# Optimization experiments

Hardware: AMD Instinct MI355X
Metric: run time of the kernel (lower is better)

The kernel has to match this reference:

```python
import jax, jax.numpy as jnp
import numpy as np

N = 50000   # nodes
E = 800000  # edges
IN, H1, H2, OUT = 128, 256, 128, 1


def setup_inputs() -> dict:
    key = jax.random.key(0)
    ks = jax.random.split(key, 9)
    x = jax.random.normal(ks[0], (N, IN), dtype=jnp.float32)
    edge_index = jax.random.randint(ks[1], (2, E), 0, N, dtype=jnp.int32)
    def glorot(k, fan_in, fan_out):
        s = np.sqrt(6.0 / (fan_in + fan_out)).astype(np.float32)
        return jax.random.uniform(k, (fan_in, fan_out), jnp.float32, -s, s)
    W1 = glorot(ks[2], IN, H1)
    b1 = jnp.zeros((H1,), jnp.float32)
    W2 = glorot(ks[3], H1, H2)
    b2 = jnp.zeros((H2,), jnp.float32)
    W3 = glorot(ks[4], H2, OUT)
    b3 = jnp.zeros((OUT,), jnp.float32)
    return {"x": x, "edge_index": edge_index, "W1": W1, "b1": b1,
            "W2": W2, "b2": b2, "W3": W3, "b3": b3}


def _gcn_layer(x, W, b, src, dst, norm):
    # dense transform [N, d_in] @ [d_in, d_out]
    h = x @ W
    # degree-normalized sparse aggregation: out[dst] += norm * h[src]
    agg = jax.ops.segment_sum(h[src] * norm[:, None], dst, num_segments=N)
    return agg + b


def reference(x, edge_index, W1, b1, W2, b2, W3, b3):
    src, dst = edge_index[0], edge_index[1]
    # PyG GCNConv: add self loops, then symmetric normalization
    loop = jnp.arange(N, dtype=src.dtype)
    src = jnp.concatenate([src, loop])
    dst = jnp.concatenate([dst, loop])
    deg = jax.ops.segment_sum(jnp.ones_like(dst, jnp.float32), dst, num_segments=N)
    dis = jax.lax.rsqrt(jnp.maximum(deg, 1.0))  # deg >= 1 via self loops
    norm = dis[src] * dis[dst]  # [E+N]
    h1 = jax.nn.relu(_gcn_layer(x, W1, b1, src, dst, norm))
    h2 = jax.nn.relu(_gcn_layer(h1, W2, b2, src, dst, norm))
    y = _gcn_layer(h2, W3, b3, src, dst, norm).reshape(-1)
    return (y, h1, h2)
```

## Files before the change

### kernel.cpp

```cpp
#include <hip/hip_runtime.h>


typedef __attribute__((ext_vector_type(8))) short short8;
typedef __attribute__((ext_vector_type(4))) float f32x4;

static __device__ __forceinline__ unsigned short f2bf(float f){
  union { float f; unsigned u; } v; v.f = f;
  unsigned r = v.u + 0x7FFF + ((v.u >> 16) & 1);
  return (unsigned short)(r >> 16);
}
static __device__ __forceinline__ float2 bf2f2(unsigned u){
  union { unsigned u; float f; } a, b;
  a.u = u << 16; b.u = u & 0xffff0000u;
  return make_float2(a.f, b.f);
}

__global__ void k_prep(const float* __restrict__ W1, const float* __restrict__ W2,
                       unsigned short* __restrict__ Wf1, unsigned short* __restrict__ Wf2,
                       const float4* __restrict__ x, uint2* __restrict__ xb, int nv,
                       int* __restrict__ bcur){
  int blk = blockIdx.x;
  int tid = threadIdx.x;
  if (blk < 256){
    if (blk == 0) bcur[tid] = 0;
    int t = blk*256 + tid;
    if (t < 32768){
      int j = t & 7, lane = (t>>3) & 63, kt = (t>>9) & 3, nt = t >> 11;
      int nn = nt*16 + (lane & 15);
      int kk = kt*32 + (lane>>4)*8 + j;
      Wf1[t] = f2bf(W1[kk*256 + nn]);
    } else {
      int o = t - 32768;
      int j = o & 7, lane = (o>>3) & 63, nt = (o>>9) & 7, kt = o >> 12;
      int nn = nt*16 + (lane & 15);
      int kk = kt*32 + (lane>>4)*8 + j;
      Wf2[o] = f2bf(W2[kk*128 + nn]);
    }
  } else {
    int i = (blk - 256)*256 + tid;
    if (i < nv){
      float4 v = x[i];
      xb[i] = make_uint2((unsigned)f2bf(v.x) | ((unsigned)f2bf(v.y) << 16),
                         (unsigned)f2bf(v.z) | ((unsigned)f2bf(v.w) << 16));
    }
  }
}

__global__ __launch_bounds__(256) void k_bin(
    const int* __restrict__ src, const int* __restrict__ dst,
    int* __restrict__ bcur, unsigned* __restrict__ pairs, int E){
  __shared__ int cl[256];
  int t = threadIdx.x;
  int e0 = blockIdx.x * 4096 + t;
  cl[t] = 0; __syncthreads();
  #pragma unroll
  for (int i = 0; i < 16; i++){
    int e = e0 + i*256;
    if (e < E) atomicAdd(&cl[dst[e] >> 8], 1);
  }
  __syncthreads();
  int c = cl[t];
  int g = (c > 0) ? atomicAdd(&bcur[t], c) : 0;
  cl[t] = g;
  __syncthreads();
  #pragma unroll
  for (int i = 0; i < 16; i++){
    int e = e0 + i*256;
    if (e < E){
      int d = dst[e];
      int b = d >> 8;
      int p = atomicAdd(&cl[b], 1);
      pairs[(b << 13) + p] = (unsigned)src[e] | ((unsigned)(d & 255) << 16);
    }
  }
}

__global__ __launch_bounds__(256) void k_place(
    const int* __restrict__ bcur, const unsigned* __restrict__ pairs,
    unsigned short* __restrict__ csr_src, int* __restrict__ rowptr,
    int* __restrict__ cnt, float* __restrict__ dis, int n, int nb){
  __shared__ int sh[256];
  __shared__ int ncnt[256];
  int t = threadIdx.x;
  int b = blockIdx.x;
  int v = (t < nb) ? bcur[t] : 0;
  sh[t] = v; __syncthreads();
  for (int off = 1; off < 256; off <<= 1){
    int x = (t >= off) ? sh[t-off] : 0;
    __syncthreads(); sh[t] += x; __syncthreads();
  }
  int csr_base = (b == 0) ? 0 : sh[b-1];
  int cnt_b = bcur[b];
  ncnt[t] = 0; __syncthreads();
  const unsigned* P = pairs + ((size_t)b << 13);
  for (int i = t; i < cnt_b; i += 256) atomicAdd(&ncnt[P[i] >> 16], 1);
  __syncthreads();
  int c = ncnt[t];
  sh[t] = c; __syncthreads();
  for (int off = 1; off < 256; off <<= 1){
    int x = (t >= off) ? sh[t-off] : 0;
    __syncthreads(); sh[t] += x; __syncthreads();
  }
  int noff = sh[t] - c;
  int node = (b << 8) + t;
  if (node < n){
    rowptr[node] = csr_base + noff;
    cnt[node] = c;
    dis[node] = rsqrtf((float)(c + 1));
  }
  ncnt[t] = noff; __syncthreads();
  for (int i = t; i < cnt_b; i += 256){
    unsigned u = P[i];
    int p = atomicAdd(&ncnt[u >> 16], 1);
    csr_src[csr_base + p] = (unsigned short)(u & 0xffff);
  }
}

__global__ void k_aggL1(const unsigned* __restrict__ xb, unsigned* __restrict__ out,
                        const int* __restrict__ rowptr, const int* __restrict__ cnt,
                        const unsigned short* __restrict__ csr_src,
                        const float* __restrict__ dis, int n){
  int t = threadIdx.x;
  int lane = t & 63;
  int node = blockIdx.x*4 + (t >> 6);
  if (node >= n) return;
  float di = dis[node];
  float2 v = bf2f2(xb[(size_t)node*64 + lane]);
  float2 acc = make_float2(di*v.x, di*v.y);
  int start = rowptr[node];
  int mm = cnt[node];
  int j = 0;
  for (; j + 15 < mm; j += 16){
    int s[16]; unsigned uv[16]; float w[16];
    #pragma unroll
    for (int q = 0; q < 16; q++) s[q] = csr_src[start+j+q];
    #pragma unroll
    for (int q = 0; q < 16; q++){ w[q] = dis[s[q]]; uv[q] = xb[(size_t)s[q]*64 + lane]; }
    #pragma unroll
    for (int q = 0; q < 16; q++){
      float2 u = bf2f2(uv[q]);
      acc.x = fmaf(w[q], u.x, acc.x); acc.y = fmaf(w[q], u.y, acc.y);
    }
  }
  for (; j + 3 < mm; j += 4){
    int s[4]; unsigned uv[4]; float w[4];
    #pragma unroll
    for (int q = 0; q < 4; q++) s[q] = csr_src[start+j+q];
    #pragma unroll
    for (int q = 0; q < 4; q++){ w[q] = dis[s[q]]; uv[q] = xb[(size_t)s[q]*64 + lane]; }
    #pragma unroll
    for (int q = 0; q < 4; q++){
      float2 u = bf2f2(uv[q]);
      acc.x = fmaf(w[q], u.x, acc.x); acc.y = fmaf(w[q], u.y, acc.y);
    }
  }
  for (; j < mm; j++){
    int s = csr_src[start+j];
    float2 u = bf2f2(xb[(size_t)s*64 + lane]);
    float w = dis[s];
    acc.x = fmaf(w, u.x, acc.x); acc.y = fmaf(w, u.y, acc.y);
  }
  acc.x *= di; acc.y *= di;
  out[(size_t)node*64 + lane] =
      (unsigned)f2bf(acc.x) | ((unsigned)f2bf(acc.y) << 16);
}

__global__ void k_aggL2(const unsigned* __restrict__ t2b, float* __restrict__ h2,
                        const int* __restrict__ rowptr, const int* __restrict__ cnt,
                        const unsigned short* __restrict__ csr_src,
                        const float* __restrict__ dis,
                        const float* __restrict__ b2, const float* __restrict__ W3,
                        float* __restrict__ u, int n){
  int t = threadIdx.x;
  int lane = t & 63;
  int node = blockIdx.x*4 + (t >> 6);
  if (node >= n) return;
  float di = dis[node];
  float2 v = bf2f2(t2b[(size_t)node*64 + lane]);
  float2 acc = make_float2(di*v.x, di*v.y);
  int start = rowptr[node];
  int mm = cnt[node];
  int j = 0;
  for (; j + 15 < mm; j += 16){
    int s[16]; unsigned uv[16]; float w[16];
    #pragma unroll
    for (int q = 0; q < 16; q++) s[q] = csr_src[start+j+q];
    #pragma unroll
    for (int q = 0; q < 16; q++){ w[q] = dis[s[q]]; uv[q] = t2b[(size_t)s[q]*64 + lane]; }
    #pragma unroll
    for (int q = 0; q < 16; q++){
      float2 uu = bf2f2(uv[q]);
      acc.x = fmaf(w[q], uu.x, acc.x); acc.y = fmaf(w[q], uu.y, acc.y);
    }
  }
  for (; j + 3 < mm; j += 4){
    int s[4]; unsigned uv[4]; float w[4];
    #pragma unroll
    for (int q = 0; q < 4; q++) s[q] = csr_src[start+j+q];
    #pragma unroll
    for (int q = 0; q < 4; q++){ w[q] = dis[s[q]]; uv[q] = t2b[(size_t)s[q]*64 + lane]; }
    #pragma unroll
    for (int q = 0; q < 4; q++){
      float2 uu = bf2f2(uv[q]);
      acc.x = fmaf(w[q], uu.x, acc.x); acc.y = fmaf(w[q], uu.y, acc.y);
    }
  }
  for (; j < mm; j++){
    int s = csr_src[start+j];
    float2 uu = bf2f2(t2b[(size_t)s*64 + lane]);
    float w = dis[s];
    acc.x = fmaf(w, uu.x, acc.x); acc.y = fmaf(w, uu.y, acc.y);
  }
  float2 b = ((const float2*)b2)[lane];
  acc.x = fmaxf(fmaf(di, acc.x, b.x), 0.0f);
  acc.y = fmaxf(fmaf(di, acc.y, b.y), 0.0f);
  ((float2*)h2)[(size_t)node*64 + lane] = acc;
  float up = fmaf(acc.x, W3[2*lane], acc.y * W3[2*lane+1]);
  #pragma unroll
  for (int off = 32; off > 0; off >>= 1) up += __shfl_down(up, off);
  if (lane == 0) u[node] = up;
}

__global__ __launch_bounds__(256) void k_gemm1_mfma(
    const unsigned short* __restrict__ Xa, const unsigned short* __restrict__ Wf1,
    const float* __restrict__ bias, float* __restrict__ out,
    unsigned short* __restrict__ h1b, int n)
{
  __shared__ unsigned short Wl[8*4*64*8];
  __shared__ unsigned short As[64*136];
  int t = threadIdx.x;
  int row0 = (blockIdx.x >> 1) * 64;
  int h = blockIdx.x & 1;
  {
    const float4* src = (const float4*)Wf1 + (size_t)h*2048;
    float4* dst = (float4*)Wl;
    #pragma unroll
    for (int i = 0; i < 8; i++) dst[i*256 + t] = src[i*256 + t];
  }
  {
    const float4* src = (const float4*)Xa;
    #pragma unroll
    for (int i = 0; i < 4; i++){
      int f = i*256 + t, r = f >> 4, c = f & 15;
      float4 v = make_float4(0,0,0,0);
      if (row0 + r < n) v = src[(size_t)(row0+r)*16 + c];
      *(float4*)&As[r*136 + c*8] = v;
    }
  }
  __syncthreads();
  int w = t >> 6, lane = t & 63, m = lane & 15, q = lane >> 4;
  int rbase = w*16;
  short8 af[4];
  #pragma unroll
  for (int kt = 0; kt < 4; kt++)
    af[kt] = *(const short8*)&As[(rbase + m)*136 + kt*32 + q*8];
  f32x4 acc[8];
  #pragma unroll
  for (int i = 0; i < 8; i++) acc[i] = (f32x4){0.f,0.f,0.f,0.f};
  #pragma unroll
  for (int nt = 0; nt < 8; nt++){
    #pragma unroll
    for (int kt = 0; kt < 4; kt++){
      short8 bfr = *(const short8*)&Wl[((nt*4 + kt)*64 + lane)*8];
      acc[nt] = __builtin_amdgcn_mfma_f32_16x16x32_bf16(af[kt], bfr, acc[nt], 0, 0, 0);
    }
  }
  int rowa = row0 + rbase + q*4;
  int colb = h*128 + m;
  #pragma unroll
  for (int nt = 0; nt < 8; nt++){
    float b = bias[colb + nt*16];
    #pragma unroll
    for (int r = 0; r < 4; r++){
      int rr = rowa + r;
      if (rr < n){
        float o = fmaxf(acc[nt][r] + b, 0.0f);
        out[(size_t)rr*256 + colb + nt*16] = o;
        h1b[(size_t)rr*256 + colb + nt*16] = f2bf(o);
      }
    }
  }
}

__global__ __launch_bounds__(256) void k_gemm2_mfma(
    const unsigned short* __restrict__ H1b, const unsigned short* __restrict__ Wf2,
    unsigned short* __restrict__ T2b, int n)
{
  __shared__ unsigned short Wl[4*8*64*8];
  __shared__ unsigned short As[64*136];
  int t = threadIdx.x;
  int row0 = blockIdx.x * 64;
  int w = t >> 6, lane = t & 63, m = lane & 15, q = lane >> 4;
  int rbase = w*16;
  f32x4 acc[8];
  #pragma unroll
  for (int i = 0; i < 8; i++) acc[i] = (f32x4){0.f,0.f,0.f,0.f};
  for (int p = 0; p < 2; p++){
    if (p) __syncthreads();
    {
      const float4* src = (const float4*)Wf2 + (size_t)p*2048;
      float4* dst = (float4*)Wl;
      #pragma unroll
      for (int i = 0; i < 8; i++) dst[i*256 + t] = src[i*256 + t];
    }
    {
      const float4* src = (const float4*)H1b;
      #pragma unroll
      for (int i = 0; i < 4; i++){
        int f = i*256 + t, r = f >> 4, c = f & 15;
        float4 v = make_float4(0,0,0,0);
        if (row0 + r < n) v = src[(size_t)(row0+r)*32 + p*16 + c];
        *(float4*)&As[r*136 + c*8] = v;
      }
    }
    __syncthreads();
    short8 af[4];
    #pragma unroll
    for (int kt = 0; kt < 4; kt++)
      af[kt] = *(const short8*)&As[(rbase + m)*136 + kt*32 + q*8];
    #pragma unroll
    for (int nt = 0; nt < 8; nt++){
      #pragma unroll
      for (int kt = 0; kt < 4; kt++){
        short8 bfr = *(const short8*)&Wl[((kt*8 + nt)*64 + lane)*8];
        acc[nt] = __builtin_amdgcn_mfma_f32_16x16x32_bf16(af[kt], bfr, acc[nt], 0, 0, 0);
      }
    }
  }
  int rowa = row0 + rbase + q*4;
  #pragma unroll
  for (int nt = 0; nt < 8; nt++){
    #pragma unroll
    for (int r = 0; r < 4; r++){
      int rr = rowa + r;
      if (rr < n) T2b[(size_t)rr*128 + nt*16 + m] = f2bf(acc[nt][r]);
    }
  }
}

__global__ void k_agg1d(const float* __restrict__ u, float* __restrict__ y,
                        const int* __restrict__ rowptr, const int* __restrict__ cnt,
                        const unsigned short* __restrict__ csr_src,
                        const float* __restrict__ dis,
                        const float* __restrict__ b3, int n){
  int i = blockIdx.x*256 + threadIdx.x;
  if (i >= n) return;
  float di = dis[i];
  float acc = di * u[i];
  int s0 = rowptr[i], m = cnt[i];
  for (int j = 0; j < m; j++){
    int s = csr_src[s0+j];
    acc = fmaf(dis[s], u[s], acc);
  }
  y[i] = fmaf(di, acc, b3[0]);
}

extern "C" void kernel_launch(void* const* d_in, const int* in_sizes, int n_in,
                              void* d_out, int out_size, void* d_ws, size_t ws_size,
                              hipStream_t stream){
  const float* x  = (const float*)d_in[0];
  const int*  ei  = (const int*)d_in[1];
  const float* W1 = (const float*)d_in[2];
  const float* b1 = (const float*)d_in[3];
  const float* W2 = (const float*)d_in[4];
  const float* b2 = (const float*)d_in[5];
  const float* W3 = (const float*)d_in[6];
  const float* b3 = (const float*)d_in[7];
  const int N = in_sizes[0] / 128;
  const int E = in_sizes[1] / 2;
  const int* src = ei;
  const int* dst = ei + E;
  const int NB = (N + 255) >> 8;

  char* p = (char*)d_ws;
  auto alloc = [&](size_t bytes)->char*{
    char* r = p; p += (bytes + 255) & ~(size_t)255; return r;
  };
  int*   bcur    = (int*)  alloc(256*4);
  int*   rowptr  = (int*)  alloc((size_t)N*4);
  int*   cnt     = (int*)  alloc((size_t)N*4);
  float* dis     = (float*)alloc((size_t)N*4);
  unsigned* pairs = (unsigned*)alloc((size_t)NB*8192*4);
  unsigned short* csr_src = (unsigned short*)alloc((size_t)E*2);
  unsigned* xb   = (unsigned*)alloc((size_t)N*128*2);
  unsigned* xa   = (unsigned*)alloc((size_t)N*128*2);
  unsigned short* h1b = (unsigned short*)alloc((size_t)N*256*2);
  unsigned short* t2b = (unsigned short*)alloc((size_t)N*128*2);
  float* u       = (float*)alloc((size_t)N*4);
  unsigned short* wf1 = (unsigned short*)alloc(32768*2);
  unsigned short* wf2 = (unsigned short*)alloc(32768*2);

  float* y  = (float*)d_out;
  float* h1 = y + N;
  float* h2 = h1 + (size_t)N*256;

  int bb = (E + 4095)/4096;
  int nb = (N + 255)/256;
  int xv = N*32;
  k_prep  <<<256 + (xv+255)/256, 256, 0, stream>>>(W1, W2, wf1, wf2,
                                                   (const float4*)x, (uint2*)xb, xv, bcur);
  k_bin   <<<bb, 256, 0, stream>>>(src, dst, bcur, pairs, E);
  k_place <<<NB, 256, 0, stream>>>(bcur, pairs, csr_src, rowptr, cnt, dis, N, NB);

  int ab = (N + 3)/4;
  int rb = (N + 63)/64;
  k_aggL1     <<<ab,   256, 0, stream>>>(xb, xa, rowptr, cnt, csr_src, dis, N);
  k_gemm1_mfma<<<rb*2, 256, 0, stream>>>((const unsigned short*)xa, wf1, b1, h1, h1b, N);
  k_gemm2_mfma<<<rb,   256, 0, stream>>>(h1b, wf2, t2b, N);
  k_aggL2     <<<ab,   256, 0, stream>>>((const unsigned*)t2b, h2, rowptr, cnt, csr_src, dis, b2, W3, u, N);
  k_agg1d     <<<nb,   256, 0, stream>>>(u, y, rowptr, cnt, csr_src, dis, b3, N);
}
```

Baseline: 264.0 us.

## Fuse both GEMMs into one kernel and merge prep with edge binning

Layer-1 and layer-2 dense GEMMs now run in a single kernel. The ReLU'd h1 tile stays in shared memory as bf16 and feeds the second MFMA GEMM directly, so the bf16 h1 round-trip through global memory and one launch are gone. The weight-prep/x-conversion kernel is merged with the edge-binning kernel, and bcur is zeroed with a memset. Weight fragments are now read straight from global memory instead of being staged in LDS. Each block now holds a 256-wide h1 tile and more accumulators, which raises register and LDS pressure and may lower occupancy.

```diff
diff --git a/kernel.cpp b/kernel.cpp
--- a/kernel.cpp
+++ b/kernel.cpp
@@ -15,15 +15,40 @@
   return make_float2(a.f, b.f);
 }
 
-__global__ void k_prep(const float* __restrict__ W1, const float* __restrict__ W2,
-                       unsigned short* __restrict__ Wf1, unsigned short* __restrict__ Wf2,
-                       const float4* __restrict__ x, uint2* __restrict__ xb, int nv,
-                       int* __restrict__ bcur){
+__global__ __launch_bounds__(256) void k_prepbin(
+    const int* __restrict__ src, const int* __restrict__ dst,
+    int* __restrict__ bcur, unsigned* __restrict__ pairs, int E, int binB,
+    const float* __restrict__ W1, const float* __restrict__ W2,
+    unsigned short* __restrict__ Wf1, unsigned short* __restrict__ Wf2,
+    const float4* __restrict__ x, uint2* __restrict__ xb, int nv){
+  __shared__ int cl[256];
   int blk = blockIdx.x;
   int tid = threadIdx.x;
-  if (blk < 256){
-    if (blk == 0) bcur[tid] = 0;
-    int t = blk*256 + tid;
+  if (blk < binB){
+    int e0 = blk * 4096 + tid;
+    cl[tid] = 0; __syncthreads();
+    #pragma unroll
+    for (int i = 0; i < 16; i++){
+      int e = e0 + i*256;
+      if (e < E) atomicAdd(&cl[dst[e] >> 8], 1);
+    }
+    __syncthreads();
+    int c = cl[tid];
+    int g = (c > 0) ? atomicAdd(&bcur[tid], c) : 0;
+    cl[tid] = g;
+    __syncthreads();
+    #pragma unroll
+    for (int i = 0; i < 16; i++){
+      int e = e0 + i*256;
+      if (e < E){
+        int d = dst[e];
+        int b = d >> 8;
+        int p = atomicAdd(&cl[b], 1);
+        pairs[(b << 13) + p] = (unsigned)src[e] | ((unsigned)(d & 255) << 16);
+      }
+    }
+  } else if (blk < binB + 256){
+    int t = (blk - binB)*256 + tid;
     if (t < 32768){
       int j = t & 7, lane = (t>>3) & 63, kt = (t>>9) & 3, nt = t >> 11;
       int nn = nt*16 + (lane & 15);
@@ -37,40 +62,11 @@
       Wf2[o] = f2bf(W2[kk*128 + nn]);
     }
   } else {
-    int i = (blk - 256)*256 + tid;
+    int i = (blk - binB - 256)*256 + tid;
     if (i < nv){
       float4 v = x[i];
       xb[i] = make_uint2((unsigned)f2bf(v.x) | ((unsigned)f2bf(v.y) << 16),
                          (unsigned)f2bf(v.z) | ((unsigned)f2bf(v.w) << 16));
-    }
-  }
-}
-
-__global__ __launch_bounds__(256) void k_bin(
-    const int* __restrict__ src, const int* __restrict__ dst,
-    int* __restrict__ bcur, unsigned* __restrict__ pairs, int E){
-  __shared__ int cl[256];
-  int t = threadIdx.x;
-  int e0 = blockIdx.x * 4096 + t;
-  cl[t] = 0; __syncthreads();
-  #pragma unroll
-  for (int i = 0; i < 16; i++){
-    int e = e0 + i*256;
-    if (e < E) atomicAdd(&cl[dst[e] >> 8], 1);
-  }
-  __syncthreads();
-  int c = cl[t];
-  int g = (c > 0) ? atomicAdd(&bcur[t], c) : 0;
-  cl[t] = g;
-  __syncthreads();
-  #pragma unroll
-  for (int i = 0; i < 16; i++){
-    int e = e0 + i*256;
-    if (e < E){
-      int d = dst[e];
-      int b = d >> 8;
-      int p = atomicAdd(&cl[b], 1);
-      pairs[(b << 13) + p] = (unsigned)src[e] | ((unsigned)(d & 255) << 16);
     }
   }
 }
@@ -221,22 +217,19 @@
   if (lane == 0) u[node] = up;
 }
 
-__global__ __launch_bounds__(256) void k_gemm1_mfma(
-    const unsigned short* __restrict__ Xa, const unsigned short* __restrict__ Wf1,
-    const float* __restrict__ bias, float* __restrict__ out,
-    unsigned short* __restrict__ h1b, int n)
+__global__ __launch_bounds__(256) void k_gemm12(
+    const unsigned short* __restrict__ Xa,
+    const unsigned short* __restrict__ Wf1,
+    const unsigned short* __restrict__ Wf2,
+    const float* __restrict__ b1,
+    float* __restrict__ h1,
+    unsigned short* __restrict__ T2b,
+    int n)
 {
-  __shared__ unsigned short Wl[8*4*64*8];
-  __shared__ unsigned short As[64*136];
+  __shared__ unsigned short As1[64*136];
+  __shared__ unsigned short As2[64*264];
   int t = threadIdx.x;
-  int row0 = (blockIdx.x >> 1) * 64;
-  int h = blockIdx.x & 1;
-  {
-    const float4* src = (const float4*)Wf1 + (size_t)h*2048;
-    float4* dst = (float4*)Wl;
-    #pragma unroll
-    for (int i = 0; i < 8; i++) dst[i*256 + t] = src[i*256 + t];
-  }
+  int row0 = blockIdx.x * 64;
   {
     const float4* src = (const float4*)Xa;
     #pragma unroll
@@ -244,7 +237,7 @@
       int f = i*256 + t, r = f >> 4, c = f & 15;
       float4 v = make_float4(0,0,0,0);
       if (row0 + r < n) v = src[(size_t)(row0+r)*16 + c];
-      *(float4*)&As[r*136 + c*8] = v;
+      *(float4*)&As1[r*136 + c*8] = v;
     }
   }
   __syncthreads();
@@ -253,87 +246,54 @@
   short8 af[4];
   #pragma unroll
   for (int kt = 0; kt < 4; kt++)
-    af[kt] = *(const short8*)&As[(rbase + m)*136 + kt*32 + q*8];
-  f32x4 acc[8];
-  #pragma unroll
-  for (int i = 0; i < 8; i++) acc[i] = (f32x4){0.f,0.f,0.f,0.f};
-  #pragma unroll
-  for (int nt = 0; nt < 8; nt++){
+    af[kt] = *(const short8*)&As1[(rbase + m)*136 + kt*32 + q*8];
+  f32x4 acc1[16];
+  #pragma unroll
+  for (int i = 0; i < 16; i++) acc1[i] = (f32x4){0.f,0.f,0.f,0.f};
+  const short8* W1v = (const short8*)Wf1;
+  #pragma unroll
+  for (int nt = 0; nt < 16; nt++){
     #pragma unroll
     for (int kt = 0; kt < 4; kt++){
-      short8 bfr = *(const short8*)&Wl[((nt*4 + kt)*64 + lane)*8];
-      acc[nt] = __builtin_amdgcn_mfma_f32_16x16x32_bf16(af[kt], bfr, acc[nt], 0, 0, 0);
+      short8 bfr = W1v[(nt*4 + kt)*64 + lane];
+      acc1[nt] = __builtin_amdgcn_mfma_f32_16x16x32_bf16(af[kt], bfr, acc1[nt], 0, 0, 0);
     }
   }
   int rowa = row0 + rbase + q*4;
-  int colb = h*128 + m;
-  #pragma unroll
-  for (int nt = 0; nt < 8; nt++){
-    float b = bias[colb + nt*16];
+  #pragma unroll
+  for (int nt = 0; nt < 16; nt++){
+    float b = b1[nt*16 + m];
     #pragma unroll
     for (int r = 0; r < 4; r++){
       int rr = rowa + r;
-      if (rr < n){
-        float o = fmaxf(acc[nt][r] + b, 0.0f);
-        out[(size_t)rr*256 + colb + nt*16] = o;
-        h1b[(size_t)rr*256 + colb + nt*16] = f2bf(o);
-      }
-    }
-  }
-}
-
-__global__ __launch_bounds__(256) void k_gemm2_mfma(
-    const unsigned short* __restrict__ H1b, const unsigned short* __restrict__ Wf2,
-    unsigned short* __restrict__ T2b, int n)
-{
-  __shared__ unsigned short Wl[4*8*64*8];
-  __shared__ unsigned short As[64*136];
-  int t = threadIdx.x;
-  int row0 = blockIdx.x * 64;
-  int w = t >> 6, lane = t & 63, m = lane & 15, q = lane >> 4;
-  int rbase = w*16;
-  f32x4 acc[8];
-  #pragma unroll
-  for (int i = 0; i < 8; i++) acc[i] = (f32x4){0.f,0.f,0.f,0.f};
-  for (int p = 0; p < 2; p++){
-    if (p) __syncthreads();
-    {
-      const float4* src = (const float4*)Wf2 + (size_t)p*2048;
-      float4* dst = (float4*)Wl;
-      #pragma unroll
-      for (int i = 0; i < 8; i++) dst[i*256 + t] = src[i*256 + t];
-    }
-    {
-      const float4* src = (const float4*)H1b;
-      #pragma unroll
-      for (int i = 0; i < 4; i++){
-        int f = i*256 + t, r = f >> 4, c = f & 15;
-        float4 v = make_float4(0,0,0,0);
-        if (row0 + r < n) v = src[(size_t)(row0+r)*32 + p*16 + c];
-        *(float4*)&As[r*136 + c*8] = v;
-      }
-    }
-    __syncthreads();
-    short8 af[4];
-    #pragma unroll
-    for (int kt = 0; kt < 4; kt++)
-      af[kt] = *(const short8*)&As[(rbase + m)*136 + kt*32 + q*8];
-    #pragma unroll
-    for (int nt = 0; nt < 8; nt++){
-      #pragma unroll
-      for (int kt = 0; kt < 4; kt++){
-        short8 bfr = *(const short8*)&Wl[((kt*8 + nt)*64 + lane)*8];
-        acc[nt] = __builtin_amdgcn_mfma_f32_16x16x32_bf16(af[kt], bfr, acc[nt], 0, 0, 0);
-      }
-    }
-  }
-  int rowa = row0 + rbase + q*4;
+      float o = fmaxf(acc1[nt][r] + b, 0.0f);
+      if (rr < n) h1[(size_t)rr*256 + nt*16 + m] = o;
+      As2[(rbase + q*4 + r)*264 + nt*16 + m] = f2bf(o);
+    }
+  }
+  __syncthreads();
+  short8 af2[8];
+  #pragma unroll
+  for (int kt = 0; kt < 8; kt++)
+    af2[kt] = *(const short8*)&As2[(rbase + m)*264 + kt*32 + q*8];
+  f32x4 acc2[8];
+  #pragma unroll
+  for (int i = 0; i < 8; i++) acc2[i] = (f32x4){0.f,0.f,0.f,0.f};
+  const short8* W2v = (const short8*)Wf2;
+  #pragma unroll
+  for (int nt = 0; nt < 8; nt++){
+    #pragma unroll
+    for (int kt = 0; kt < 8; kt++){
+      short8 bfr = W2v[(kt*8 + nt)*64 + lane];
+      acc2[nt] = __builtin_amdgcn_mfma_f32_16x16x32_bf16(af2[kt], bfr, acc2[nt], 0, 0, 0);
+    }
+  }
   #pragma unroll
   for (int nt = 0; nt < 8; nt++){
     #pragma unroll
     for (int r = 0; r < 4; r++){
       int rr = rowa + r;
-      if (rr < n) T2b[(size_t)rr*128 + nt*16 + m] = f2bf(acc[nt][r]);
+      if (rr < n) T2b[(size_t)rr*128 + nt*16 + m] = f2bf(acc2[nt][r]);
     }
   }
 }
@@ -384,7 +344,6 @@
   unsigned short* csr_src = (unsigned short*)alloc((size_t)E*2);
   unsigned* xb   = (unsigned*)alloc((size_t)N*128*2);
   unsigned* xa   = (unsigned*)alloc((size_t)N*128*2);
-  unsigned short* h1b = (unsigned short*)alloc((size_t)N*256*2);
   unsigned short* t2b = (unsigned short*)alloc((size_t)N*128*2);
   float* u       = (float*)alloc((size_t)N*4);
   unsigned short* wf1 = (unsigned short*)alloc(32768*2);
@@ -397,16 +356,18 @@
   int bb = (E + 4095)/4096;
   int nb = (N + 255)/256;
   int xv = N*32;
-  k_prep  <<<256 + (xv+255)/256, 256, 0, stream>>>(W1, W2, wf1, wf2,
-                                                   (const float4*)x, (uint2*)xb, xv, bcur);
-  k_bin   <<<bb, 256, 0, stream>>>(src, dst, bcur, pairs, E);
-  k_place <<<NB, 256, 0, stream>>>(bcur, pairs, csr_src, rowptr, cnt, dis, N, NB);
+  int xblk = (xv + 255)/256;
+
+  hipMemsetAsync(bcur, 0, 256*4, stream);
+  k_prepbin <<<bb + 256 + xblk, 256, 0, stream>>>(
+      src, dst, bcur, pairs, E, bb, W1, W2, wf1, wf2,
+      (const float4*)x, (uint2*)xb, xv);
+  k_place   <<<NB, 256, 0, stream>>>(bcur, pairs, csr_src, rowptr, cnt, dis, N, NB);
 
   int ab = (N + 3)/4;
   int rb = (N + 63)/64;
-  k_aggL1     <<<ab,   256, 0, stream>>>(xb, xa, rowptr, cnt, csr_src, dis, N);
-  k_gemm1_mfma<<<rb*2, 256, 0, stream>>>((const unsigned short*)xa, wf1, b1, h1, h1b, N);
-  k_gemm2_mfma<<<rb,   256, 0, stream>>>(h1b, wf2, t2b, N);
-  k_aggL2     <<<ab,   256, 0, stream>>>((const unsigned*)t2b, h2, rowptr, cnt, csr_src, dis, b2, W3, u, N);
-  k_agg1d     <<<nb,   256, 0, stream>>>(u, y, rowptr, cnt, csr_src, dis, b3, N);
-}
+  k_aggL1   <<<ab, 256, 0, stream>>>(xb, xa, rowptr, cnt, csr_src, dis, N);
+  k_gemm12  <<<rb, 256, 0, stream>>>((const unsigned short*)xa, wf1, wf2, b1, h1, t2b, N);
+  k_aggL2   <<<ab, 256, 0, stream>>>((const unsigned*)t2b, h2, rowptr, cnt, csr_src, dis, b2, W3, u, N);
+  k_agg1d   <<<nb, 256, 0, stream>>>(u, y, rowptr, cnt, csr_src, dis, b3, N);
+}
```

After: 274.3 us. 1.04x slower.
